# Performance work log

Hardware: AMD Instinct MI355X
Metric: run time of the kernel (lower is better)

## Reference

```python
import jax, jax.numpy as jnp
import numpy as np

N, IN_DIM, OUT_DIM, HEADS = 8192, 256, 128, 2


def setup_inputs() -> dict:
    key = jax.random.key(0)
    k1, k2, k3, k4, k5 = jax.random.split(key, 5)
    features = jax.random.normal(k1, (N, IN_DIM), dtype=jnp.float32)
    adjacency = jax.random.randint(k2, (N, N), 0, 2, dtype=jnp.int32)
    # nn.Linear(input_dim, output_dim*heads, bias=False): weight [out, in]
    W = jax.random.normal(k3, (OUT_DIM * HEADS, IN_DIM), dtype=jnp.float32) * 0.05
    attn_src = jax.random.normal(k4, (HEADS, OUT_DIM), dtype=jnp.float32) * 0.05
    attn_dst = jax.random.normal(k5, (HEADS, OUT_DIM), dtype=jnp.float32) * 0.05
    return {"features": features, "adjacency": adjacency, "W": W,
            "attn_src": attn_src, "attn_dst": attn_dst}


def reference(features, adjacency, W, attn_src, attn_dst):
    n = features.shape[0]
    # transformed: [N, H, F]
    transformed = (features @ W.T).reshape(n, HEADS, OUT_DIM)
    src_scores = jnp.einsum('nhf,hf->nh', transformed, attn_src)  # [N, H]
    dst_scores = jnp.einsum('nhf,hf->nh', transformed, attn_dst)  # [N, H]
    # logits: [N_src, N_dst, H]
    logits = jax.nn.leaky_relu(src_scores[:, None, :] + dst_scores[None, :, :],
                               negative_slope=0.2)
    mask = adjacency > 0  # [N, N]
    logits = jnp.where(mask[:, :, None], logits, -jnp.inf)
    attention = jax.nn.softmax(logits, axis=1)  # softmax over dst dim (dim=1)
    attention = jnp.nan_to_num(attention, nan=0.0, posinf=0.0, neginf=0.0)
    aggregated = jnp.einsum('ijh,jhf->ihf', attention, transformed)  # [N, H, F]
    return aggregated.mean(axis=1)  # [N, F]
```

## Files before the change

### kernel.cpp

```cpp
#include <hip/hip_runtime.h>
#include <stdint.h>
#include <stddef.h>

#define NN 8192
#define KD 256
#define CD 256
#define FD 128
#define BI 32
#define BJ 32
#define PACK_BLOCKS 512

typedef __attribute__((ext_vector_type(4))) float f32x4;
typedef __attribute__((ext_vector_type(8))) short b16x8;

__device__ __forceinline__ unsigned short f2bf(float x) {
    unsigned int u = __float_as_uint(x);
    u += 0x7fffu + ((u >> 16) & 1u);
    return (unsigned short)(u >> 16);
}

__device__ __forceinline__ void async16(const void* g, void* l) {
    __builtin_amdgcn_global_load_lds(
        (const __attribute__((address_space(1))) unsigned int*)g,
        (__attribute__((address_space(3))) unsigned int*)l, 16, 0, 0);
}

__device__ __forceinline__ float wsel_store(
    int m8, const float4 f0, const float4 f1, const float4 h0, const float4 h1,
    float Ei, float Gi, unsigned short* wdst)
{
    const float ff[8] = {f0.x, f0.y, f0.z, f0.w, f1.x, f1.y, f1.z, f1.w};
    const float hh[8] = {h0.x, h0.y, h0.z, h0.w, h1.x, h1.y, h1.z, h1.w};
    float e[8]; float dp = 0.f;
#pragma unroll
    for (int k = 0; k < 8; ++k) {
        float w = fmaxf(Ei * ff[k], Gi * hh[k]);
        w = (m8 & (1 << k)) ? w : 0.f;
        dp += w; e[k] = w;
    }
    union { unsigned short us[8]; b16x8 v; } pk;
#if __has_builtin(__builtin_amdgcn_cvt_pk_bf16_f32)
#pragma unroll
    for (int k = 0; k < 4; ++k) {
        auto p = __builtin_amdgcn_cvt_pk_bf16_f32(e[2 * k], e[2 * k + 1]);
        __builtin_memcpy(&pk.us[2 * k], &p, 4);
    }
#else
#pragma unroll
    for (int k = 0; k < 8; ++k) pk.us[k] = f2bf(e[k]);
#endif
    *(b16x8*)wdst = pk.v;
    return dp;
}

__global__ __launch_bounds__(256) void k_front(
    const float* __restrict__ feat, const float* __restrict__ W,
    const float* __restrict__ asrc, const float* __restrict__ adst,
    const int* __restrict__ adj, unsigned char* __restrict__ MT,
    unsigned short* __restrict__ TB,
    float* __restrict__ SE, float* __restrict__ SG,
    float* __restrict__ SF, float* __restrict__ SH)
{
    __shared__ unsigned short a_lds[64 * 32];
    __shared__ unsigned short b_lds[256 * 32];
    __shared__ unsigned short tr_lds[256 * 72];
    __shared__ float sc_lds[4][64];
    __shared__ float dc_lds[4][64];
    __shared__ unsigned char pk_lds[1024 * 16];

    const int t = threadIdx.x;

    if (blockIdx.x >= 128) {
        const int pb = blockIdx.x - 128;
        const int I = pb >> 1, half = pb & 1;
        const int row_base = I * 32 + half * 16;
        const int4* a4 = (const int4*)adj;
#pragma unroll 4
        for (int st = 0; st < 128; ++st) {
            const int g = st * 256 + t;
            const int row16 = g >> 11;
            const int j4 = g & 2047;
            const int4 v = a4[(size_t)(row_base + row16) * 2048 + j4];
            unsigned int nib = (v.x != 0 ? 1u : 0u) | (v.y != 0 ? 2u : 0u) |
                               (v.z != 0 ? 4u : 0u) | (v.w != 0 ? 8u : 0u);
            unsigned int b = nib << (4 * (t & 1));
            b |= __shfl_xor(b, 1);
            if ((t & 1) == 0) pk_lds[(j4 >> 1) * 16 + row16] = (unsigned char)b;
        }
        __syncthreads();
        unsigned int* mt32 = (unsigned int*)MT;
        const unsigned int* src = (const unsigned int*)pk_lds;
        for (int i = 0; i < 16; ++i) {
            const int w = i * 256 + t;
            const int jb = w >> 2, r4 = w & 3;
            mt32[(size_t)I * 8192 + jb * 8 + half * 4 + r4] = src[w];
        }
        return;
    }

    const int wave = t >> 6, lane = t & 63;
    const int l15 = lane & 15, quad = lane >> 4;
    const int n0 = blockIdx.x * 64;
    const int ai = t >> 2, ag = t & 3;

    f32x4 acc[4][4] = {};
    for (int kc = 0; kc < 8; ++kc) {
        const int k0 = kc * 32;
        __syncthreads();
        {
            const float* src = feat + (size_t)(n0 + ai) * KD + k0 + ag * 8;
            const float4 v0 = *(const float4*)src;
            const float4 v1 = *(const float4*)(src + 4);
            union { unsigned short us[8]; b16x8 v; } pk;
            pk.us[0] = f2bf(v0.x); pk.us[1] = f2bf(v0.y);
            pk.us[2] = f2bf(v0.z); pk.us[3] = f2bf(v0.w);
            pk.us[4] = f2bf(v1.x); pk.us[5] = f2bf(v1.y);
            pk.us[6] = f2bf(v1.z); pk.us[7] = f2bf(v1.w);
            const int slot = ag ^ ((ai >> 1) & 3);
            *(b16x8*)&a_lds[ai * 32 + slot * 8] = pk.v;
        }
        for (int p = 0; p < 4; ++p) {
            const int G = p * 256 + t;
            const int c = G >> 2, g = G & 3;
            const float* src = W + (size_t)c * KD + k0 + g * 8;
            const float4 v0 = *(const float4*)src;
            const float4 v1 = *(const float4*)(src + 4);
            union { unsigned short us[8]; b16x8 v; } pk;
            pk.us[0] = f2bf(v0.x); pk.us[1] = f2bf(v0.y);
            pk.us[2] = f2bf(v0.z); pk.us[3] = f2bf(v0.w);
            pk.us[4] = f2bf(v1.x); pk.us[5] = f2bf(v1.y);
            pk.us[6] = f2bf(v1.z); pk.us[7] = f2bf(v1.w);
            const int slot = g ^ ((c >> 1) & 3);
            *(b16x8*)&b_lds[c * 32 + slot * 8] = pk.v;
        }
        __syncthreads();
        b16x8 af[4], bfr[4];
        for (int mt = 0; mt < 4; ++mt) {
            const int m = mt * 16 + l15;
            af[mt] = *(const b16x8*)&a_lds[m * 32 + (quad ^ ((m >> 1) & 3)) * 8];
        }
        for (int nt = 0; nt < 4; ++nt) {
            const int c = wave * 64 + nt * 16 + l15;
            bfr[nt] = *(const b16x8*)&b_lds[c * 32 + (quad ^ ((c >> 1) & 3)) * 8];
        }
        for (int mt = 0; mt < 4; ++mt)
            for (int nt = 0; nt < 4; ++nt)
                acc[mt][nt] = __builtin_amdgcn_mfma_f32_16x16x32_bf16(
                    af[mt], bfr[nt], acc[mt][nt], 0, 0, 0);
    }

    float aS[4], aD[4];
    for (int nt = 0; nt < 4; ++nt) {
        const int c = wave * 64 + nt * 16 + l15;
        aS[nt] = asrc[c]; aD[nt] = adst[c];
    }
    for (int mt = 0; mt < 4; ++mt)
        for (int r = 0; r < 4; ++r) {
            float vs = 0.f, vd = 0.f;
            for (int nt = 0; nt < 4; ++nt) {
                const float x = acc[mt][nt][r];
                vs += x * aS[nt]; vd += x * aD[nt];
            }
            vs += __shfl_xor(vs, 1); vd += __shfl_xor(vd, 1);
            vs += __shfl_xor(vs, 2); vd += __shfl_xor(vd, 2);
            vs += __shfl_xor(vs, 4); vd += __shfl_xor(vd, 4);
            vs += __shfl_xor(vs, 8); vd += __shfl_xor(vd, 8);
            if (l15 == 0) {
                const int nl = mt * 16 + quad * 4 + r;
                sc_lds[wave][nl] = vs; dc_lds[wave][nl] = vd;
            }
        }
    for (int mt = 0; mt < 4; ++mt)
        for (int nt = 0; nt < 4; ++nt)
            for (int r = 0; r < 4; ++r) {
                const int c = wave * 64 + nt * 16 + l15;
                const int n = mt * 16 + quad * 4 + r;
                tr_lds[c * 72 + n] = f2bf(acc[mt][nt][r]);
            }
    __syncthreads();
    if (t < 128) {
        const int n = t >> 1, h = t & 1;
        const float s = sc_lds[h * 2][n] + sc_lds[h * 2 + 1][n];
        const float d = dc_lds[h * 2][n] + dc_lds[h * 2 + 1][n];
        SE[(size_t)h * NN + n0 + n] = __expf(s);
        SG[(size_t)h * NN + n0 + n] = __expf(0.2f * s);
        SF[(size_t)h * NN + n0 + n] = __expf(d);
        SH[(size_t)h * NN + n0 + n] = __expf(0.2f * d);
    }
    for (int p = 0; p < 8; ++p) {
        const int idx = p * 256 + t;
        const int c = idx >> 3, g = idx & 7;
        unsigned short* dst = TB + ((size_t)((n0 >> 5) + (g >> 2))) * 8192
                              + c * 32 + (g & 3) * 8;
        *(b16x8*)dst = *(const b16x8*)&tr_lds[c * 72 + g * 8];
    }
}

__global__ __launch_bounds__(256, 4) void k_gat(
    const unsigned char* __restrict__ MT, const unsigned short* __restrict__ TB,
    const float* __restrict__ SE, const float* __restrict__ SG,
    const float* __restrict__ SF, const float* __restrict__ SH,
    float* __restrict__ num_part,
    float* __restrict__ den_part,
    int njt)
{
    __shared__ unsigned short tt_lds[2][256 * 32];
    __shared__ unsigned short w_lds[2][2][32][32];

    const int t = threadIdx.x;
    const int wave = t >> 6, lane = t & 63;
    const int l15 = lane & 15, quad = lane >> 4;
    const int i0 = blockIdx.x * BI;
    const int chunk = blockIdx.y;
    const size_t jbase = (size_t)chunk * njt * BJ;

    const int eh = t >> 7;
    const int wi = (t >> 2) & 31;
    const int g4 = t & 3;
    const int gi = i0 + wi;
    const float Ei = SE[(size_t)eh * NN + gi];
    const float Gi = SG[(size_t)eh * NN + gi];
    const int wslot = (g4 ^ (wi & 3) ^ ((wi >> 2) & 3)) * 8;

    const int mh = wave >> 1, fh = wave & 1;
    const int cb = mh * 128 + fh * 64;

    f32x4 acc[2][4] = {};
    float den = 0.f;

    const unsigned short* tb0 = TB + (jbase >> 5) * 8192;
    const unsigned char* mrow = MT + ((size_t)(i0 >> 5)) * 32768
                                + (jbase >> 3) * 32 + g4 * 32 + wi;
    const float* fp = SF + (size_t)eh * NN + jbase + g4 * 8;
    const float* hp = SH + (size_t)eh * NN + jbase + g4 * 8;

    for (int p = 0; p < 4; ++p) {
        const int G = (p * 4 + wave) * 64 + lane;
        const int c = G >> 2;
        const int g = (G & 3) ^ ((c >> 1) & 3);
        async16(tb0 + (size_t)c * 32 + g * 8,
                (char*)&tt_lds[0][0] + (size_t)(p * 4 + wave) * 1024);
    }
    __builtin_amdgcn_sched_barrier(0);
    int cM = mrow[0];
    float4 cF0 = *(const float4*)(fp),     cF1 = *(const float4*)(fp + 4);
    float4 cH0 = *(const float4*)(hp),     cH1 = *(const float4*)(hp + 4);
    int nM; float4 nF0, nF1, nH0, nH1;
    {
        const int j1 = (njt > 1) ? 1 : 0;
        nM = mrow[j1 * 128];
        nF0 = *(const float4*)(fp + j1 * BJ); nF1 = *(const float4*)(fp + j1 * BJ + 4);
        nH0 = *(const float4*)(hp + j1 * BJ); nH1 = *(const float4*)(hp + j1 * BJ + 4);
        den += wsel_store(cM, cF0, cF1, cH0, cH1, Ei, Gi, &w_lds[0][eh][wi][wslot]);
        cM = nM; cF0 = nF0; cF1 = nF1; cH0 = nH0; cH1 = nH1;
    }
    asm volatile("s_waitcnt vmcnt(5) lgkmcnt(0)\n\ts_barrier" ::: "memory");

    for (int jt = 0; jt < njt; ++jt) {
        const int cur = jt & 1, nxt = cur ^ 1;
        b16x8 af[2], bfr[4];
        for (int mt = 0; mt < 2; ++mt) {
            const int m = mt * 16 + l15;
            af[mt] = *(const b16x8*)
                &w_lds[cur][mh][m][(quad ^ (m & 3) ^ ((m >> 2) & 3)) * 8];
        }
        for (int nt = 0; nt < 4; ++nt) {
            const int c = cb + nt * 16 + l15;
            bfr[nt] = *(const b16x8*)&tt_lds[cur][c * 32 + (quad ^ ((c >> 1) & 3)) * 8];
        }
        const unsigned short* tbn = tb0 + (size_t)((jt + 1 < njt) ? jt + 1 : jt) * 8192;
        for (int p = 0; p < 4; ++p) {
            const int G = (p * 4 + wave) * 64 + lane;
            const int c = G >> 2;
            const int g = (G & 3) ^ ((c >> 1) & 3);
            async16(tbn + (size_t)c * 32 + g * 8,
                    (char*)&tt_lds[nxt][0] + (size_t)(p * 4 + wave) * 1024);
        }
        __builtin_amdgcn_sched_barrier(0);
        const int j2 = (jt + 2 < njt) ? jt + 2 : njt - 1;
        nM = mrow[j2 * 128];
        nF0 = *(const float4*)(fp + j2 * BJ); nF1 = *(const float4*)(fp + j2 * BJ + 4);
        nH0 = *(const float4*)(hp + j2 * BJ); nH1 = *(const float4*)(hp + j2 * BJ + 4);
        const float dpv = wsel_store(cM, cF0, cF1, cH0, cH1, Ei, Gi,
                                     &w_lds[nxt][eh][wi][wslot]);
        if (jt + 1 < njt) den += dpv;
        for (int mt = 0; mt < 2; ++mt)
            for (int nt = 0; nt < 4; ++nt)
                acc[mt][nt] = __builtin_amdgcn_mfma_f32_16x16x32_bf16(
                    af[mt], bfr[nt], acc[mt][nt], 0, 0, 0);
        cM = nM; cF0 = nF0; cF1 = nF1; cH0 = nH0; cH1 = nH1;
        asm volatile("s_waitcnt vmcnt(5) lgkmcnt(0)\n\ts_barrier" ::: "memory");
    }

    float dv = den;
    dv += __shfl_xor(dv, 1); dv += __shfl_xor(dv, 2);
    if (g4 == 0)
        den_part[((size_t)chunk * 2 + eh) * NN + gi] = dv;

    float* np_ = num_part + (size_t)chunk * NN * CD;
    for (int mt = 0; mt < 2; ++mt)
        for (int nt = 0; nt < 4; ++nt)
            for (int r = 0; r < 4; ++r) {
                const int n = i0 + mt * 16 + quad * 4 + r;
                const int c = cb + nt * 16 + l15;
                np_[(size_t)n * CD + c] = acc[mt][nt][r];
            }
}

__global__ __launch_bounds__(256) void k_combine(
    const float* __restrict__ num_part, const float* __restrict__ den_part,
    float* __restrict__ out, int jsplit)
{
    const int idx = blockIdx.x * 256 + threadIdx.x;
    const int n = idx >> 7, f = idx & 127;
    const size_t row = (size_t)n * CD;
    float n0 = 0.f, n1 = 0.f, d0 = 0.f, d1 = 0.f;
    for (int c = 0; c < jsplit; ++c) {
        const size_t base = (size_t)c * NN * CD;
        n0 += num_part[base + row + f];
        n1 += num_part[base + row + 128 + f];
        d0 += den_part[((size_t)c * 2 + 0) * NN + n];
        d1 += den_part[((size_t)c * 2 + 1) * NN + n];
    }
    const float r0 = d0 != 0.f ? n0 / d0 : 0.f;
    const float r1 = d1 != 0.f ? n1 / d1 : 0.f;
    out[idx] = 0.5f * (r0 + r1);
}

extern "C" void kernel_launch(void* const* d_in, const int* in_sizes, int n_in,
                              void* d_out, int out_size, void* d_ws, size_t ws_size,
                              hipStream_t stream) {
    const float* feat = (const float*)d_in[0];
    const int*   adj  = (const int*)d_in[1];
    const float* W    = (const float*)d_in[2];
    const float* asrc = (const float*)d_in[3];
    const float* adst = (const float*)d_in[4];
    float* out = (float*)d_out;

    const int jsplit = (ws_size >= ((size_t)45 << 20)) ? 4 : 2;
    const int njt = (NN / jsplit) / BJ;

    char* ws = (char*)d_ws;
    unsigned short* TB = (unsigned short*)ws;
    float* SE = (float*)(ws + ((size_t)4 << 20));
    float* SG = (float*)(ws + ((size_t)4 << 20) + (64 << 10));
    float* SF = (float*)(ws + ((size_t)4 << 20) + (128 << 10));
    float* SH = (float*)(ws + ((size_t)4 << 20) + (192 << 10));
    float* den = (float*)(ws + ((size_t)4 << 20) + (256 << 10));
    unsigned char* MT = (unsigned char*)(ws + ((size_t)5 << 20));
    float* nump = (float*)(ws + ((size_t)13 << 20));

    k_front<<<128 + PACK_BLOCKS, 256, 0, stream>>>(feat, W, asrc, adst, adj,
                                                   MT, TB, SE, SG, SF, SH);
    k_gat<<<dim3(NN / BI, jsplit), 256, 0, stream>>>(MT, TB, SE, SG, SF, SH,
                                                     nump, den, njt);
    k_combine<<<NN * FD / 256, 256, 0, stream>>>(nump, den, out, jsplit);
}
```

Baseline: 502.1 us.

## Load MFMA fragments directly from global memory, drop LDS staging and barriers

The GAT aggregation kernel no longer stages the transformed-feature tile and the attention-weight tile through LDS. Each wave now loads its B fragments straight from global memory and builds its own A fragments (masked exp weights) in registers, with software double-buffering (A/B register sets) instead of async global-to-LDS copies and block barriers. Blocks grow to 512 threads covering 64 rows so that adjacent waves share TB reads through cache. This removes LDS traffic and synchronisation, but each wave now recomputes the weight fragments redundantly across the fh halves and depends on L1/L2 for reuse of TB, with higher register pressure.

Result: slower. 525.8 us (+4.7%).

```diff
diff --git a/kernel.cpp b/kernel.cpp
--- a/kernel.cpp
+++ b/kernel.cpp
@@ -6,8 +6,7 @@
 #define KD 256
 #define CD 256
 #define FD 128
-#define BI 32
-#define BJ 32
+#define BI 64
 #define PACK_BLOCKS 512
 
 typedef __attribute__((ext_vector_type(4))) float f32x4;
@@ -19,15 +18,9 @@
     return (unsigned short)(u >> 16);
 }
 
-__device__ __forceinline__ void async16(const void* g, void* l) {
-    __builtin_amdgcn_global_load_lds(
-        (const __attribute__((address_space(1))) unsigned int*)g,
-        (__attribute__((address_space(3))) unsigned int*)l, 16, 0, 0);
-}
-
-__device__ __forceinline__ float wsel_store(
+__device__ __forceinline__ float wsel_frag(
     int m8, const float4 f0, const float4 f1, const float4 h0, const float4 h1,
-    float Ei, float Gi, unsigned short* wdst)
+    float Ei, float Gi, b16x8* out)
 {
     const float ff[8] = {f0.x, f0.y, f0.z, f0.w, f1.x, f1.y, f1.z, f1.w};
     const float hh[8] = {h0.x, h0.y, h0.z, h0.w, h1.x, h1.y, h1.z, h1.w};
@@ -49,7 +42,7 @@
 #pragma unroll
     for (int k = 0; k < 8; ++k) pk.us[k] = f2bf(e[k]);
 #endif
-    *(b16x8*)wdst = pk.v;
+    *out = pk.v;
     return dp;
 }
 
@@ -196,7 +189,7 @@
     }
 }
 
-__global__ __launch_bounds__(256, 4) void k_gat(
+__global__ __launch_bounds__(512, 4) void k_gat(
     const unsigned char* __restrict__ MT, const unsigned short* __restrict__ TB,
     const float* __restrict__ SE, const float* __restrict__ SG,
     const float* __restrict__ SF, const float* __restrict__ SH,
@@ -204,102 +197,95 @@
     float* __restrict__ den_part,
     int njt)
 {
-    __shared__ unsigned short tt_lds[2][256 * 32];
-    __shared__ unsigned short w_lds[2][2][32][32];
-
     const int t = threadIdx.x;
     const int wave = t >> 6, lane = t & 63;
     const int l15 = lane & 15, quad = lane >> 4;
-    const int i0 = blockIdx.x * BI;
+    const int fh = wave & 1, mh = (wave >> 1) & 1, ih = wave >> 2;
+    const int i0 = blockIdx.x * BI + ih * 32;
     const int chunk = blockIdx.y;
-    const size_t jbase = (size_t)chunk * njt * BJ;
-
-    const int eh = t >> 7;
-    const int wi = (t >> 2) & 31;
-    const int g4 = t & 3;
-    const int gi = i0 + wi;
-    const float Ei = SE[(size_t)eh * NN + gi];
-    const float Gi = SG[(size_t)eh * NN + gi];
-    const int wslot = (g4 ^ (wi & 3) ^ ((wi >> 2) & 3)) * 8;
-
-    const int mh = wave >> 1, fh = wave & 1;
+    const size_t jbase = (size_t)chunk * njt * 32;
     const int cb = mh * 128 + fh * 64;
 
+    const float Ei0 = SE[(size_t)mh * NN + i0 + l15];
+    const float Ei1 = SE[(size_t)mh * NN + i0 + 16 + l15];
+    const float Gi0 = SG[(size_t)mh * NN + i0 + l15];
+    const float Gi1 = SG[(size_t)mh * NN + i0 + 16 + l15];
+
+    const unsigned short* tbL = TB + (jbase >> 5) * 8192 + (size_t)(cb + l15) * 32 + quad * 8;
+    const unsigned char*  mL  = MT + ((size_t)(i0 >> 5)) * 32768 + (jbase >> 3) * 32
+                                 + quad * 32 + l15;
+    const float* fp = SF + (size_t)mh * NN + jbase + quad * 8;
+    const float* hp = SH + (size_t)mh * NN + jbase + quad * 8;
+
     f32x4 acc[2][4] = {};
-    float den = 0.f;
-
-    const unsigned short* tb0 = TB + (jbase >> 5) * 8192;
-    const unsigned char* mrow = MT + ((size_t)(i0 >> 5)) * 32768
-                                + (jbase >> 3) * 32 + g4 * 32 + wi;
-    const float* fp = SF + (size_t)eh * NN + jbase + g4 * 8;
-    const float* hp = SH + (size_t)eh * NN + jbase + g4 * 8;
-
-    for (int p = 0; p < 4; ++p) {
-        const int G = (p * 4 + wave) * 64 + lane;
-        const int c = G >> 2;
-        const int g = (G & 3) ^ ((c >> 1) & 3);
-        async16(tb0 + (size_t)c * 32 + g * 8,
-                (char*)&tt_lds[0][0] + (size_t)(p * 4 + wave) * 1024);
-    }
-    __builtin_amdgcn_sched_barrier(0);
-    int cM = mrow[0];
-    float4 cF0 = *(const float4*)(fp),     cF1 = *(const float4*)(fp + 4);
-    float4 cH0 = *(const float4*)(hp),     cH1 = *(const float4*)(hp + 4);
-    int nM; float4 nF0, nF1, nH0, nH1;
-    {
-        const int j1 = (njt > 1) ? 1 : 0;
-        nM = mrow[j1 * 128];
-        nF0 = *(const float4*)(fp + j1 * BJ); nF1 = *(const float4*)(fp + j1 * BJ + 4);
-        nH0 = *(const float4*)(hp + j1 * BJ); nH1 = *(const float4*)(hp + j1 * BJ + 4);
-        den += wsel_store(cM, cF0, cF1, cH0, cH1, Ei, Gi, &w_lds[0][eh][wi][wslot]);
-        cM = nM; cF0 = nF0; cF1 = nF1; cH0 = nH0; cH1 = nH1;
-    }
-    asm volatile("s_waitcnt vmcnt(5) lgkmcnt(0)\n\ts_barrier" ::: "memory");
-
-    for (int jt = 0; jt < njt; ++jt) {
-        const int cur = jt & 1, nxt = cur ^ 1;
-        b16x8 af[2], bfr[4];
-        for (int mt = 0; mt < 2; ++mt) {
-            const int m = mt * 16 + l15;
-            af[mt] = *(const b16x8*)
-                &w_lds[cur][mh][m][(quad ^ (m & 3) ^ ((m >> 2) & 3)) * 8];
-        }
-        for (int nt = 0; nt < 4; ++nt) {
-            const int c = cb + nt * 16 + l15;
-            bfr[nt] = *(const b16x8*)&tt_lds[cur][c * 32 + (quad ^ ((c >> 1) & 3)) * 8];
-        }
-        const unsigned short* tbn = tb0 + (size_t)((jt + 1 < njt) ? jt + 1 : jt) * 8192;
-        for (int p = 0; p < 4; ++p) {
-            const int G = (p * 4 + wave) * 64 + lane;
-            const int c = G >> 2;
-            const int g = (G & 3) ^ ((c >> 1) & 3);
-            async16(tbn + (size_t)c * 32 + g * 8,
-                    (char*)&tt_lds[nxt][0] + (size_t)(p * 4 + wave) * 1024);
-        }
-        __builtin_amdgcn_sched_barrier(0);
-        const int j2 = (jt + 2 < njt) ? jt + 2 : njt - 1;
-        nM = mrow[j2 * 128];
-        nF0 = *(const float4*)(fp + j2 * BJ); nF1 = *(const float4*)(fp + j2 * BJ + 4);
-        nH0 = *(const float4*)(hp + j2 * BJ); nH1 = *(const float4*)(hp + j2 * BJ + 4);
-        const float dpv = wsel_store(cM, cF0, cF1, cH0, cH1, Ei, Gi,
-                                     &w_lds[nxt][eh][wi][wslot]);
-        if (jt + 1 < njt) den += dpv;
-        for (int mt = 0; mt < 2; ++mt)
-            for (int nt = 0; nt < 4; ++nt)
-                acc[mt][nt] = __builtin_amdgcn_mfma_f32_16x16x32_bf16(
-                    af[mt], bfr[nt], acc[mt][nt], 0, 0, 0);
-        cM = nM; cF0 = nF0; cF1 = nF1; cH0 = nH0; cH1 = nH1;
-        asm volatile("s_waitcnt vmcnt(5) lgkmcnt(0)\n\ts_barrier" ::: "memory");
-    }
-
-    float dv = den;
-    dv += __shfl_xor(dv, 1); dv += __shfl_xor(dv, 2);
-    if (g4 == 0)
-        den_part[((size_t)chunk * 2 + eh) * NN + gi] = dv;
+    float den0 = 0.f, den1 = 0.f;
+
+    int   mA0, mA1, mB0, mB1;
+    float4 fA0, fA1, hA0, hA1, fB0, fB1, hB0, hB1;
+    b16x8 bA[4], bB[4];
+
+    mA0 = mL[0]; mA1 = mL[16];
+    fA0 = *(const float4*)(fp);     fA1 = *(const float4*)(fp + 4);
+    hA0 = *(const float4*)(hp);     hA1 = *(const float4*)(hp + 4);
+#pragma unroll
+    for (int nt = 0; nt < 4; ++nt) bA[nt] = *(const b16x8*)(tbL + nt * 512);
+
+    for (int jt = 0; jt < njt; jt += 2) {
+        {
+            const int jn = jt + 1;
+            mB0 = mL[jn * 128]; mB1 = mL[jn * 128 + 16];
+            fB0 = *(const float4*)(fp + jn * 32); fB1 = *(const float4*)(fp + jn * 32 + 4);
+            hB0 = *(const float4*)(hp + jn * 32); hB1 = *(const float4*)(hp + jn * 32 + 4);
+#pragma unroll
+            for (int nt = 0; nt < 4; ++nt)
+                bB[nt] = *(const b16x8*)(tbL + (size_t)jn * 8192 + nt * 512);
+            b16x8 a0, a1;
+            den0 += wsel_frag(mA0, fA0, fA1, hA0, hA1, Ei0, Gi0, &a0);
+            den1 += wsel_frag(mA1, fA0, fA1, hA0, hA1, Ei1, Gi1, &a1);
+#pragma unroll
+            for (int nt = 0; nt < 4; ++nt)
+                acc[0][nt] = __builtin_amdgcn_mfma_f32_16x16x32_bf16(
+                    a0, bA[nt], acc[0][nt], 0, 0, 0);
+#pragma unroll
+            for (int nt = 0; nt < 4; ++nt)
+                acc[1][nt] = __builtin_amdgcn_mfma_f32_16x16x32_bf16(
+                    a1, bA[nt], acc[1][nt], 0, 0, 0);
+        }
+        {
+            const int jn = (jt + 2 < njt) ? jt + 2 : njt - 1;
+            mA0 = mL[jn * 128]; mA1 = mL[jn * 128 + 16];
+            fA0 = *(const float4*)(fp + jn * 32); fA1 = *(const float4*)(fp + jn * 32 + 4);
+            hA0 = *(const float4*)(hp + jn * 32); hA1 = *(const float4*)(hp + jn * 32 + 4);
+#pragma unroll
+            for (int nt = 0; nt < 4; ++nt)
+                bA[nt] = *(const b16x8*)(tbL + (size_t)jn * 8192 + nt * 512);
+            b16x8 a0, a1;
+            den0 += wsel_frag(mB0, fB0, fB1, hB0, hB1, Ei0, Gi0, &a0);
+            den1 += wsel_frag(mB1, fB0, fB1, hB0, hB1, Ei1, Gi1, &a1);
+#pragma unroll
+            for (int nt = 0; nt < 4; ++nt)
+                acc[0][nt] = __builtin_amdgcn_mfma_f32_16x16x32_bf16(
+                    a0, bB[nt], acc[0][nt], 0, 0, 0);
+#pragma unroll
+            for (int nt = 0; nt < 4; ++nt)
+                acc[1][nt] = __builtin_amdgcn_mfma_f32_16x16x32_bf16(
+                    a1, bB[nt], acc[1][nt], 0, 0, 0);
+        }
+    }
+
+    den0 += __shfl_xor(den0, 16); den0 += __shfl_xor(den0, 32);
+    den1 += __shfl_xor(den1, 16); den1 += __shfl_xor(den1, 32);
+    if (fh == 0 && quad == 0) {
+        den_part[((size_t)chunk * 2 + mh) * NN + i0 + l15] = den0;
+        den_part[((size_t)chunk * 2 + mh) * NN + i0 + 16 + l15] = den1;
+    }
 
     float* np_ = num_part + (size_t)chunk * NN * CD;
+#pragma unroll
     for (int mt = 0; mt < 2; ++mt)
+#pragma unroll
         for (int nt = 0; nt < 4; ++nt)
+#pragma unroll
             for (int r = 0; r < 4; ++r) {
                 const int n = i0 + mt * 16 + quad * 4 + r;
                 const int c = cb + nt * 16 + l15;
@@ -338,7 +324,7 @@
     float* out = (float*)d_out;
 
     const int jsplit = (ws_size >= ((size_t)45 << 20)) ? 4 : 2;
-    const int njt = (NN / jsplit) / BJ;
+    const int njt = (NN / jsplit) / 32;
 
     char* ws = (char*)d_ws;
     unsigned short* TB = (unsigned short*)ws;
@@ -352,7 +338,7 @@
 
     k_front<<<128 + PACK_BLOCKS, 256, 0, stream>>>(feat, W, asrc, adst, adj,
                                                    MT, TB, SE, SG, SF, SH);
-    k_gat<<<dim3(NN / BI, jsplit), 256, 0, stream>>>(MT, TB, SE, SG, SF, SH,
+    k_gat<<<dim3(NN / BI, jsplit), 512, 0, stream>>>(MT, TB, SE, SG, SF, SH,
                                                      nump, den, njt);
     k_combine<<<NN * FD / 256, 256, 0, stream>>>(nump, den, out, jsplit);
 }
```
